# Optimization experiments

Measured on AMD Instinct MI355X. Metric: run time of the kernel, lower is better.

Reference implementation:

```python
import jax, jax.numpy as jnp
import numpy as np
from jax import lax

SCALE = 2
UP_K = 5  # reassembly kernel
ENC_K = 3


def conv2d(x, w, padding):
    # x: (N,C,H,W), w: (O,I,kh,kw)
    return lax.conv_general_dilated(
        x, w, window_strides=(1, 1), padding=[(padding, padding)] * 2,
        dimension_numbers=("NCHW", "OIHW", "NCHW"))


def pixel_shuffle(x, r):
    # (N, C*r*r, H, W) -> (N, C, r*H, r*W), matching torch.nn.functional.pixel_shuffle
    N, Crr, H, W = x.shape
    C = Crr // (r * r)
    x = x.reshape(N, C, r, r, H, W)
    x = x.transpose(0, 1, 4, 2, 5, 3)  # N, C, H, r, W, r
    return x.reshape(N, C, H * r, W * r)


def setup_inputs() -> dict:
    key = jax.random.key(0)
    k1, k2, k3, k4 = jax.random.split(key, 4)
    N, C, H, W = 2, 256, 64, 64
    comp = 64
    enc_out = UP_K * UP_K * SCALE * SCALE  # 100
    features = jax.random.normal(k1, (N, C, H, W), dtype=jnp.float32)
    w_comp = jax.random.normal(k2, (comp, C, 1, 1), dtype=jnp.float32) * (1.0 / np.sqrt(C))
    b_comp = jax.random.normal(k3, (comp,), dtype=jnp.float32) * 0.01
    w_enc = jax.random.normal(k4, (enc_out, comp, ENC_K, ENC_K), dtype=jnp.float32) * 0.001
    return {"features": features, "w_comp": w_comp, "b_comp": b_comp, "w_enc": w_enc}


def carafe_forward(features, w_comp, b_comp, w_enc):
    N, C, H, W = features.shape
    r = SCALE
    # 1) channel compression (1x1 conv + bias; norm_type=None)
    compressed = conv2d(features, w_comp, padding=0) + b_comp[None, :, None, None]
    # 2) content encoding -> (N, k^2 * r^2, H, W)
    kp = conv2d(compressed, w_enc, padding=(ENC_K - 1) // 2)
    # pixel shuffle -> (N, k^2, rH, rW)
    kp = pixel_shuffle(kp, r)
    # 3) softmax over the k^2 kernel dim
    kernels = jax.nn.softmax(kp, axis=1)  # (N, k2, sH, sW)
    # 4) nearest-neighbor upsample
    feat_up = jnp.repeat(jnp.repeat(features, r, axis=2), r, axis=3)  # (N,C,sH,sW)
    sH, sW = H * r, W * r
    pad = (UP_K // 2) * r  # unfold padding, dilation = r
    xpad = jnp.pad(feat_up, ((0, 0), (0, 0), (pad, pad), (pad, pad)))
    # accumulate the softmax-weighted gather over the k x k dilated neighborhood
    out = jnp.zeros((N, C, sH, sW), dtype=features.dtype)
    for i in range(UP_K):
        for j in range(UP_K):
            patch = xpad[:, :, i * r:i * r + sH, j * r:j * r + sW]  # (N,C,sH,sW)
            wgt = kernels[:, i * UP_K + j]  # (N,sH,sW)
            out = out + patch * wgt[:, None, :, :]
    return out


def reference(features, w_comp, b_comp, w_enc):
    return carafe_forward(features, w_comp, b_comp, w_enc)
```

## Files before the change

kernel.cpp:

```cpp
#include <hip/hip_runtime.h>
#include <hip/hip_bf16.h>
#include <math.h>

#define CIN 256

typedef __attribute__((ext_vector_type(8))) short short8v;
typedef __attribute__((ext_vector_type(4))) float f32x4;


__device__ inline ushort f2bf(float x) {
    __hip_bfloat16 b = __float2bfloat16(x);
    return *reinterpret_cast<ushort*>(&b);
}

__device__ inline float dpp_shl1(float x) {
    int r = __builtin_amdgcn_update_dpp(0, __builtin_bit_cast(int, x), 0x130, 0xf, 0xf, true);
    return __builtin_bit_cast(float, r);
}
__device__ inline float dpp_shr1(float x) {
    int r = __builtin_amdgcn_update_dpp(0, __builtin_bit_cast(int, x), 0x138, 0xf, 0xf, true);
    return __builtin_bit_cast(float, r);
}

__global__ __launch_bounds__(256) void prep_compress(const float* __restrict__ w_comp,
                                                     const float* __restrict__ w_enc,
                                                     const float* __restrict__ b_comp,
                                                     const float* __restrict__ feat,
                                                     ushort* __restrict__ Bsw,
                                                     ushort* __restrict__ compB) {
    int bid = blockIdx.x, tid = threadIdx.x;
    if (bid >= 256) {
        int i = (bid - 256) * 256 + tid;
        int j = i & 7, lane = (i >> 3) & 63, rest = i >> 9;
        int nf = rest & 7, ks = rest >> 3;
        int ct = ks >> 1, dh = ct / 3, dw = ct % 3;
        int cc = (ks & 1) * 32 + (lane >> 4) * 8 + j;
        int o  = nf * 16 + (lane & 15);
        float v = (o < 100) ? w_enc[((o * 64 + cc) * 3 + dh) * 3 + dw] : 0.f;
        Bsw[i] = f2bf(v);
        return;
    }
    __shared__ ushort at[32][264];
    int p0 = bid * 32;
    int n = p0 >> 12, hw0 = p0 & 4095;
    const float* fb = feat + (size_t)n * CIN * 4096 + hw0;
    {
        int p4 = tid & 7, cr = tid >> 3;
        #pragma unroll
        for (int k = 0; k < 8; ++k) {
            int c = cr + k * 32;
            float4 v = *reinterpret_cast<const float4*>(fb + (size_t)c * 4096 + p4 * 4);
            at[p4 * 4 + 0][c] = f2bf(v.x);
            at[p4 * 4 + 1][c] = f2bf(v.y);
            at[p4 * 4 + 2][c] = f2bf(v.z);
            at[p4 * 4 + 3][c] = f2bf(v.w);
        }
    }
    __syncthreads();
    int lane = tid & 63, nf = tid >> 6;
    int lr = lane & 15, lk = lane >> 4;
    int cc = nf * 16 + lr;
    f32x4 acc0 = {0, 0, 0, 0}, acc1 = {0, 0, 0, 0};
    const float* wrow = w_comp + (size_t)cc * 256;
    #pragma unroll
    for (int ks = 0; ks < 8; ++ks) {
        float4 b0 = *reinterpret_cast<const float4*>(wrow + ks * 32 + lk * 8);
        float4 b1 = *reinterpret_cast<const float4*>(wrow + ks * 32 + lk * 8 + 4);
        short8v b;
        b[0] = (short)f2bf(b0.x); b[1] = (short)f2bf(b0.y);
        b[2] = (short)f2bf(b0.z); b[3] = (short)f2bf(b0.w);
        b[4] = (short)f2bf(b1.x); b[5] = (short)f2bf(b1.y);
        b[6] = (short)f2bf(b1.z); b[7] = (short)f2bf(b1.w);
        short8v a0 = *reinterpret_cast<const short8v*>(&at[lr][ks * 32 + lk * 8]);
        short8v a1 = *reinterpret_cast<const short8v*>(&at[16 + lr][ks * 32 + lk * 8]);
        acc0 = __builtin_amdgcn_mfma_f32_16x16x32_bf16(a0, b, acc0, 0, 0, 0);
        acc1 = __builtin_amdgcn_mfma_f32_16x16x32_bf16(a1, b, acc1, 0, 0, 0);
    }
    float bv = b_comp[cc];
    #pragma unroll
    for (int i = 0; i < 4; ++i) {
        compB[(size_t)(p0 + lk * 4 + i) * 64 + cc]      = f2bf(acc0[i] + bv);
        compB[(size_t)(p0 + 16 + lk * 4 + i) * 64 + cc] = f2bf(acc1[i] + bv);
    }
}

__global__ __launch_bounds__(512) void enc_gemm_softmax(const ushort* __restrict__ compB,
                                                        const ushort* __restrict__ Bsw,
                                                        float* __restrict__ wgt) {
    int p0 = blockIdx.x * 16;
    int n = p0 >> 12, h = (p0 >> 6) & 63, w0 = p0 & 63;
    int tid = threadIdx.x, lane = tid & 63, nf = tid >> 6;
    int lr = lane & 15, lk = lane >> 4;
    int wpix = w0 + lr;
    f32x4 acc = {0, 0, 0, 0};
    #pragma unroll
    for (int ks = 0; ks < 18; ++ks) {
        int ct = ks >> 1, dh = ct / 3, dw = ct - dh * 3;
        int hh = h + dh - 1;
        if ((unsigned)hh >= 64u) continue;
        int ww = wpix + dw - 1;
        short8v a = {};
        if ((unsigned)ww < 64u)
            a = *reinterpret_cast<const short8v*>(
                    compB + ((size_t)(n * 4096 + hh * 64 + ww) * 64 + (ks & 1) * 32 + lk * 8));
        short8v b = *reinterpret_cast<const short8v*>(
                    Bsw + ((size_t)(ks * 8 + nf) * 64 + lane) * 8);
        acc = __builtin_amdgcn_mfma_f32_16x16x32_bf16(a, b, acc, 0, 0, 0);
    }
    __shared__ float kp_lds[16][132];
    __shared__ float kp2[100][17];
    #pragma unroll
    for (int i = 0; i < 4; ++i)
        kp_lds[lk * 4 + i][nf * 16 + lr] = acc[i];
    __syncthreads();
    if (tid < 64) {
        int pl = tid & 15, sub = tid >> 4;
        float v[25], mx = -1e30f;
        #pragma unroll
        for (int t = 0; t < 25; ++t) { v[t] = kp_lds[pl][t * 4 + sub]; mx = fmaxf(mx, v[t]); }
        float s = 0.f;
        #pragma unroll
        for (int t = 0; t < 25; ++t) { v[t] = __expf(v[t] - mx); s += v[t]; }
        float inv = 1.f / s;
        #pragma unroll
        for (int t = 0; t < 25; ++t) kp2[sub * 25 + t][pl] = v[t] * inv;
    }
    __syncthreads();
    {
        int pl = tid & 15, r0 = tid >> 4;
        float* wb = wgt + (size_t)((n * 64 + h)) * 6400 + w0 + pl;
        #pragma unroll
        for (int it = 0; it < 4; ++it) {
            int r = it * 32 + r0;
            if (r < 100) wb[r * 64] = kp2[r][pl];
        }
    }
}

__global__ __launch_bounds__(256, 4) void apply_v3(const float* __restrict__ feat,
                                                   const float* __restrict__ wgt,
                                                   float* __restrict__ out) {
    int bid = blockIdx.x;
    int wgid = (bid & 7) * 128 + (bid >> 3);
    int cg = wgid & 7;
    int nh = wgid >> 3;
    int n = nh >> 6, h = nh & 63;
    int tid = threadIdx.x;
    int w  = tid & 63;
    int ci = tid >> 6;
    int c0 = cg * 32 + ci * 8;

    __shared__ float wlds[4 * 25 * 64];
    {
        const float* wg = wgt + (size_t)nh * 6400;
        #pragma unroll
        for (int it = 0; it < 25; ++it)
            wlds[it * 256 + tid] = wg[it * 256 + tid];
    }
    __syncthreads();

    const float* fbase = feat + ((size_t)(n * CIN + c0)) * 4096;

    float acc[4][8];
    #pragma unroll
    for (int s = 0; s < 4; ++s)
        #pragma unroll
        for (int k = 0; k < 8; ++k) acc[s][k] = 0.f;

    #pragma unroll
    for (int i = 0; i < 5; ++i) {
        int hh = h + i - 2;
        if ((unsigned)hh >= 64u) continue;
        float wv[4][5];
        #pragma unroll
        for (int s = 0; s < 4; ++s)
            #pragma unroll
            for (int j = 0; j < 5; ++j)
                wv[s][j] = wlds[(s * 25 + i * 5 + j) * 64 + w];
        #pragma unroll
        for (int k = 0; k < 8; ++k) {
            float v = fbase[(size_t)k * 4096 + (hh << 6) + w];
            float vm1 = dpp_shr1(v);
            float vm2 = dpp_shr1(vm1);
            float vp1 = dpp_shl1(v);
            float vp2 = dpp_shl1(vp1);
            float fv[5] = {vm2, vm1, v, vp1, vp2};
            #pragma unroll
            for (int j = 0; j < 5; ++j)
                #pragma unroll
                for (int s = 0; s < 4; ++s)
                    acc[s][k] += fv[j] * wv[s][j];
        }
    }

    #pragma unroll
    for (int k = 0; k < 8; ++k) {
        float* o = out + ((size_t)(n * CIN + c0 + k) * 128 + 2 * h) * 128 + 2 * w;
        *reinterpret_cast<float2*>(o)       = make_float2(acc[0][k], acc[1][k]);
        *reinterpret_cast<float2*>(o + 128) = make_float2(acc[2][k], acc[3][k]);
    }
}

extern "C" void kernel_launch(void* const* d_in, const int* in_sizes, int n_in,
                              void* d_out, int out_size, void* d_ws, size_t ws_size,
                              hipStream_t stream) {
    const float* features = (const float*)d_in[0];
    const float* w_comp   = (const float*)d_in[1];
    const float* b_comp   = (const float*)d_in[2];
    const float* w_enc    = (const float*)d_in[3];
    float* out = (float*)d_out;
    float* ws  = (float*)d_ws;

    ushort* Bsw   = (ushort*)ws;
    ushort* compB = (ushort*)(ws + 36864);
    float*  wgt   = ws + 299008;

    hipLaunchKernelGGL(prep_compress, dim3(544), dim3(256), 0, stream,
                       w_comp, w_enc, b_comp, features, Bsw, compB);
    hipLaunchKernelGGL(enc_gemm_softmax, dim3(512), dim3(512), 0, stream, compB, Bsw, wgt);
    hipLaunchKernelGGL(apply_v3, dim3(1024), dim3(256), 0, stream, features, wgt, out);
}
```

Measured before the change: 35.67 us.

## Stage encoder input halo in LDS and interleave softmax weights by subpixel

The encoder GEMM kernel now loads a 3x18 pixel halo tile of compressed features into swizzled LDS once per block. Before, each MFMA step read overlapping rows directly from global memory with boundary checks. The softmax weight buffer layout changes to [tap][w][subpixel] so the apply kernel can load it with float4 copies and read each tap's four subpixel weights as one vector LDS load. The encoder kernel also gains an occupancy hint in its launch bounds, and it now writes scattered 4-byte stores to the interleaved layout.

```diff
diff --git a/kernel.cpp b/kernel.cpp
--- a/kernel.cpp
+++ b/kernel.cpp
@@ -84,29 +84,40 @@
     }
 }
 
-__global__ __launch_bounds__(512) void enc_gemm_softmax(const ushort* __restrict__ compB,
-                                                        const ushort* __restrict__ Bsw,
-                                                        float* __restrict__ wgt) {
+__global__ __launch_bounds__(512, 4) void enc_gemm_softmax(const ushort* __restrict__ compB,
+                                                           const ushort* __restrict__ Bsw,
+                                                           float* __restrict__ wgt) {
     int p0 = blockIdx.x * 16;
     int n = p0 >> 12, h = (p0 >> 6) & 63, w0 = p0 & 63;
     int tid = threadIdx.x, lane = tid & 63, nf = tid >> 6;
     int lr = lane & 15, lk = lane >> 4;
-    int wpix = w0 + lr;
+
+    __shared__ ushort ctile[3 * 18 * 64];
+    if (tid < 432) {
+        int q = tid & 7, pp = (tid >> 3) % 18, r = (tid >> 3) / 18;
+        int hh = h + r - 1, ww = w0 - 1 + pp;
+        uint4 val = {0, 0, 0, 0};
+        if ((unsigned)hh < 64u && (unsigned)ww < 64u)
+            val = *reinterpret_cast<const uint4*>(
+                compB + ((size_t)(n * 4096 + hh * 64 + ww) * 64 + q * 8));
+        *reinterpret_cast<uint4*>(&ctile[((r * 18 + pp) * 8 + (q ^ (pp & 7))) * 8]) = val;
+    }
+    __syncthreads();
+
     f32x4 acc = {0, 0, 0, 0};
     #pragma unroll
     for (int ks = 0; ks < 18; ++ks) {
-        int ct = ks >> 1, dh = ct / 3, dw = ct - dh * 3;
-        int hh = h + dh - 1;
-        if ((unsigned)hh >= 64u) continue;
-        int ww = wpix + dw - 1;
-        short8v a = {};
-        if ((unsigned)ww < 64u)
-            a = *reinterpret_cast<const short8v*>(
-                    compB + ((size_t)(n * 4096 + hh * 64 + ww) * 64 + (ks & 1) * 32 + lk * 8));
+        int ct = ks >> 1, half = ks & 1;
+        int dh = ct / 3, dw = ct - dh * 3;
+        int pp = lr + dw;
+        int q  = half * 4 + lk;
+        short8v a = *reinterpret_cast<const short8v*>(
+            &ctile[((dh * 18 + pp) * 8 + (q ^ (pp & 7))) * 8]);
         short8v b = *reinterpret_cast<const short8v*>(
-                    Bsw + ((size_t)(ks * 8 + nf) * 64 + lane) * 8);
+            Bsw + ((size_t)(ks * 8 + nf) * 64 + lane) * 8);
         acc = __builtin_amdgcn_mfma_f32_16x16x32_bf16(a, b, acc, 0, 0, 0);
     }
+
     __shared__ float kp_lds[16][132];
     __shared__ float kp2[100][17];
     #pragma unroll
@@ -127,17 +138,15 @@
     }
     __syncthreads();
     {
-        int pl = tid & 15, r0 = tid >> 4;
-        float* wb = wgt + (size_t)((n * 64 + h)) * 6400 + w0 + pl;
-        #pragma unroll
-        for (int it = 0; it < 4; ++it) {
-            int r = it * 32 + r0;
-            if (r < 100) wb[r * 64] = kp2[r][pl];
+        float* wb = wgt + (size_t)(n * 64 + h) * 6400;
+        for (int u = tid; u < 1600; u += 512) {
+            int s = u & 3, pl = (u >> 2) & 15, t = u >> 6;
+            wb[(t * 64 + w0 + pl) * 4 + s] = kp2[s * 25 + t][pl];
         }
     }
 }
 
-__global__ __launch_bounds__(256, 4) void apply_v3(const float* __restrict__ feat,
+__global__ __launch_bounds__(256, 4) void apply_v5(const float* __restrict__ feat,
                                                    const float* __restrict__ wgt,
                                                    float* __restrict__ out) {
     int bid = blockIdx.x;
@@ -150,12 +159,11 @@
     int ci = tid >> 6;
     int c0 = cg * 32 + ci * 8;
 
-    __shared__ float wlds[4 * 25 * 64];
+    __shared__ float wlds[6400];
     {
-        const float* wg = wgt + (size_t)nh * 6400;
-        #pragma unroll
-        for (int it = 0; it < 25; ++it)
-            wlds[it * 256 + tid] = wg[it * 256 + tid];
+        const float4* wg = reinterpret_cast<const float4*>(wgt + (size_t)nh * 6400);
+        float4* wl = reinterpret_cast<float4*>(wlds);
+        for (int u = tid; u < 1600; u += 256) wl[u] = wg[u];
     }
     __syncthreads();
 
@@ -171,12 +179,10 @@
     for (int i = 0; i < 5; ++i) {
         int hh = h + i - 2;
         if ((unsigned)hh >= 64u) continue;
-        float wv[4][5];
-        #pragma unroll
-        for (int s = 0; s < 4; ++s)
-            #pragma unroll
-            for (int j = 0; j < 5; ++j)
-                wv[s][j] = wlds[(s * 25 + i * 5 + j) * 64 + w];
+        f32x4 wv[5];
+        #pragma unroll
+        for (int j = 0; j < 5; ++j)
+            wv[j] = *reinterpret_cast<const f32x4*>(&wlds[((i * 5 + j) * 64 + w) * 4]);
         #pragma unroll
         for (int k = 0; k < 8; ++k) {
             float v = fbase[(size_t)k * 4096 + (hh << 6) + w];
@@ -189,7 +195,7 @@
             for (int j = 0; j < 5; ++j)
                 #pragma unroll
                 for (int s = 0; s < 4; ++s)
-                    acc[s][k] += fv[j] * wv[s][j];
+                    acc[s][k] += fv[j] * wv[j][s];
         }
     }
 
@@ -218,5 +224,5 @@
     hipLaunchKernelGGL(prep_compress, dim3(544), dim3(256), 0, stream,
                        w_comp, w_enc, b_comp, features, Bsw, compB);
     hipLaunchKernelGGL(enc_gemm_softmax, dim3(512), dim3(512), 0, stream, compB, Bsw, wgt);
-    hipLaunchKernelGGL(apply_v3, dim3(1024), dim3(256), 0, stream, features, wgt, out);
-}
+    hipLaunchKernelGGL(apply_v5, dim3(1024), dim3(256), 0, stream, features, wgt, out);
+}
```

Result: faster. 29.89 us, median of 2 (-16.2%).
